# Optimization experiments

Hardware: AMD Instinct MI355X
Metric: run time of the kernel (lower is better)

The kernel has to match this reference:

```python
import jax, jax.numpy as jnp
import numpy as np

N, F, H, C = 50000, 128, 256, 40
E = 800000
L, J = 3, 2
TOT = 7  # sum_{i<L} J**i


def setup_inputs() -> dict:
    key = jax.random.key(0)
    ks = jax.random.split(key, 16)
    def rn(k, shape, scale):
        return jax.random.normal(k, shape, jnp.float32) * scale
    w = lambda k, shape: rn(k, shape, 1.0 / np.sqrt(shape[0]).astype(np.float32))
    return {
        "x": rn(ks[0], (N, F), 1.0),
        "feature": rn(ks[1], (TOT, N, F), 1.0),
        "src": jax.random.randint(ks[2], (E,), 0, N),
        "dst": jax.random.randint(ks[3], (E,), 0, N),
        "conv_W0": w(ks[4], (F, H)),       "conv_b0": jnp.zeros((H,), jnp.float32),
        "conv_W1": w(ks[5], (2 * H, H)),   "conv_b1": jnp.zeros((H,), jnp.float32),
        "conv_W2": w(ks[6], (2 * H, H)),   "conv_b2": jnp.zeros((H,), jnp.float32),
        "lin_W0": w(ks[7], (F, H)),        "lin_b0": jnp.zeros((H,), jnp.float32),
        "lin_W1": w(ks[8], (2 * F, H)),    "lin_b1": jnp.zeros((H,), jnp.float32),
        "lin_W2": w(ks[9], (4 * F, H)),    "lin_b2": jnp.zeros((H,), jnp.float32),
        "order_weights": rn(ks[10], (J,), 1.0 / np.sqrt(J).astype(np.float32)),
        "cls_W": w(ks[11], (2 * H, C)),    "cls_b": jnp.zeros((C,), jnp.float32),
    }


def reference(x, feature, src, dst,
              conv_W0, conv_b0, conv_W1, conv_b1, conv_W2, conv_b2,
              lin_W0, lin_b0, lin_W1, lin_b1, lin_W2, lin_b2,
              order_weights, cls_W, cls_b):
    # GCN normalization with self-loops (A-hat = D^-1/2 (A+I) D^-1/2)
    loop = jnp.arange(N, dtype=src.dtype)
    src_sl = jnp.concatenate([src, loop])   # [E+N]
    dst_sl = jnp.concatenate([dst, loop])
    deg = jax.ops.segment_sum(jnp.ones_like(dst_sl, jnp.float32), dst_sl, num_segments=N)
    dinv = jax.lax.rsqrt(deg)  # deg >= 1 thanks to self loops
    norm = dinv[src_sl] * dinv[dst_sl]      # [E+N]

    def gcn(h, W, b):
        m = h @ W                            # transform first (smaller gather)
        agg = jax.ops.segment_sum(m[src_sl] * norm[:, None], dst_sl, num_segments=N)
        return agg + b

    conv_W = [conv_W0, conv_W1, conv_W2]
    conv_b = [conv_b0, conv_b1, conv_b2]
    lin_W = [lin_W0, lin_W1, lin_W2]
    lin_b = [lin_b0, lin_b1, lin_b2]

    comb = x
    begin = 0
    for i in range(L):
        convx = jax.nn.relu(gcn(comb, conv_W[i], conv_b[i]))  # [N, H]
        count = J ** i
        lf = feature[begin:begin + count]                      # [count, N, F]
        if i > 0:
            ow = jnp.tile(order_weights, J ** (i - 1)).reshape(-1, 1, 1)
            lf = ow * lf
        lf = jnp.moveaxis(lf, 0, 1).reshape(N, count * F)      # [N, count*F]
        lin_sct = jax.nn.relu(lf @ lin_W[i] + lin_b[i])        # [N, H]
        comb = jnp.concatenate([lin_sct, convx], axis=-1)      # [N, 2H]
        begin += count
    logits = gcn(comb, cls_W, cls_b)                           # [N, C]
    return jax.nn.log_softmax(logits, axis=-1), logits
```

## Files before the change

### kernel.cpp

```cpp
#include <hip/hip_runtime.h>

#define DEVI __device__ __forceinline__

namespace {

constexpr int Nn = 50000;
constexpr int Ne = 800000;
constexpr int Fd = 128;
constexpr int Hd = 256;
constexpr int Cd = 40;
constexpr int NB = (Nn + 255) / 256;

typedef __attribute__((ext_vector_type(8))) short s16x8;
typedef __attribute__((ext_vector_type(8))) unsigned short u16x8;
typedef __attribute__((ext_vector_type(4))) float f32x4;

DEVI unsigned short f2bf(float f) {
  unsigned int u = __builtin_bit_cast(unsigned int, f);
  u += 0x7fffu + ((u >> 16) & 1u);
  return (unsigned short)(u >> 16);
}
DEVI float bf2f(unsigned short s) {
  return __builtin_bit_cast(float, ((unsigned int)s) << 16);
}

DEVI void gld_lds16(const void* gptr, void* lds_base) {
  const unsigned m0v =
      (unsigned)__builtin_amdgcn_readfirstlane((unsigned)(uintptr_t)lds_base);
  asm volatile("s_mov_b32 m0, %0\n\t"
               "global_load_lds_dwordx4 %1, off"
               :: "s"(m0v), "v"(gptr) : "memory");
}

DEVI void wt_one(const float* __restrict__ W, unsigned short* __restrict__ Wt,
                 int idx, int K, int H, const float* __restrict__ ow) {
  int c = idx / K, k = idx - c * K;
  int kt = k >> 6, c16 = (k >> 3) & 7, j = k & 7;
  int ksrc = (kt << 6) | ((c16 ^ (c & 7)) << 3) | j;
  float v = (c < H) ? W[(size_t)ksrc * H + c] : 0.0f;
  if (ow) v *= ow[(ksrc >> 7) & 1];
  Wt[idx] = f2bf(v);
}

constexpr int WTO0 = 0;
constexpr int WTO1 = WTO0 + 256 * 128;
constexpr int WTO2 = WTO1 + 256 * 512;
constexpr int WTO3 = WTO2 + 256 * 512;
constexpr int WTO4 = WTO3 + 256 * 128;
constexpr int WTO5 = WTO4 + 256 * 256;
constexpr int WTO6 = WTO5 + 256 * 512;
constexpr int WTO7 = WTO6 + 64 * 512;
constexpr int PREPTOT = WTO7 + Nn;

__global__ __launch_bounds__(256) void k_prep(
    const float* W0, const float* W1, const float* W2, const float* W3,
    const float* W4, const float* W5, const float* W6, const float* ow,
    unsigned short* T0, unsigned short* T1, unsigned short* T2, unsigned short* T3,
    unsigned short* T4, unsigned short* T5, unsigned short* T6, int* cnt) {
  int idx = blockIdx.x * 256 + threadIdx.x;
  if (idx >= PREPTOT) return;
  if (idx < WTO1)      wt_one(W0, T0, idx - WTO0, 128, 256, nullptr);
  else if (idx < WTO2) wt_one(W1, T1, idx - WTO1, 512, 256, nullptr);
  else if (idx < WTO3) wt_one(W2, T2, idx - WTO2, 512, 256, nullptr);
  else if (idx < WTO4) wt_one(W3, T3, idx - WTO3, 128, 256, nullptr);
  else if (idx < WTO5) wt_one(W4, T4, idx - WTO4, 256, 256, ow);
  else if (idx < WTO6) wt_one(W5, T5, idx - WTO5, 512, 256, ow);
  else if (idx < WTO7) wt_one(W6, T6, idx - WTO6, 512, 40, nullptr);
  else cnt[idx - WTO7] = 0;
}

__global__ void k_count(const int* __restrict__ dst, int* __restrict__ cnt) {
  int e = blockIdx.x * 256 + threadIdx.x;
  if (e < Ne) atomicAdd(&cnt[dst[e]], 1);
}

__global__ __launch_bounds__(256) void k_partial(const int* __restrict__ cnt,
                                                 int* __restrict__ partial) {
  __shared__ int red[256];
  const int t = threadIdx.x;
  const int i = blockIdx.x * 256 + t;
  red[t] = (i < Nn) ? cnt[i] + 1 : 0;
  __syncthreads();
#pragma unroll
  for (int off = 128; off; off >>= 1) {
    if (t < off) red[t] += red[t + off];
    __syncthreads();
  }
  if (t == 0) partial[blockIdx.x] = red[0];
}

__global__ __launch_bounds__(256) void k_scan_small(const int* __restrict__ partial,
                                                    int* __restrict__ poffs,
                                                    int* __restrict__ rowptr) {
  __shared__ int s[256];
  const int t = threadIdx.x;
  const int v = (t < NB) ? partial[t] : 0;
  s[t] = v;
  __syncthreads();
#pragma unroll
  for (int off = 1; off < 256; off <<= 1) {
    int add = (t >= off) ? s[t - off] : 0;
    __syncthreads();
    s[t] += add;
    __syncthreads();
  }
  if (t < NB) poffs[t] = s[t] - v;
  if (t == NB - 1) rowptr[Nn] = s[t];
}

__global__ __launch_bounds__(256) void k_rowptr(const int* __restrict__ cnt,
                                                const int* __restrict__ poffs,
                                                int* __restrict__ rowptr,
                                                int* __restrict__ cursor,
                                                float* __restrict__ dinv) {
  __shared__ int s[256];
  const int t = threadIdx.x;
  const int i = blockIdx.x * 256 + t;
  const int c = (i < Nn) ? cnt[i] + 1 : 0;
  s[t] = c;
  __syncthreads();
#pragma unroll
  for (int off = 1; off < 256; off <<= 1) {
    int add = (t >= off) ? s[t - off] : 0;
    __syncthreads();
    s[t] += add;
    __syncthreads();
  }
  if (i < Nn) {
    const int excl = s[t] - c + poffs[blockIdx.x];
    rowptr[i] = excl;
    cursor[i] = excl;
    dinv[i] = rsqrtf((float)c);
  }
}

__global__ void k_fill(const int* __restrict__ src, const int* __restrict__ dst,
                       const float* __restrict__ dinv, int* __restrict__ cursor,
                       int* __restrict__ csrs, float* __restrict__ csrn) {
  int e = blockIdx.x * 256 + threadIdx.x;
  if (e < Ne) {
    int s = src[e], d = dst[e];
    int pos = atomicAdd(&cursor[d], 1);
    csrs[pos] = s;
    csrn[pos] = dinv[s] * dinv[d];
  } else if (e < Ne + Nn) {
    int d = e - Ne;
    int pos = atomicAdd(&cursor[d], 1);
    csrs[pos] = d;
    float v = dinv[d];
    csrn[pos] = v * v;
  }
}

struct GRole {
  const float* A;
  const unsigned short* Wt;
  const float* bias;
  unsigned short* C;
  int K;
  int ldc;
  int relu;
};

__global__ __launch_bounds__(256) void k_gemm4(GRole R0, GRole R1, GRole R2, GRole R3) {
  const GRole R = (blockIdx.y == 0) ? R0 : (blockIdx.y == 1) ? R1
                  : (blockIdx.y == 2) ? R2 : R3;
  __shared__ char smem[81920];
  short* lA0 = (short*)smem;
  short* lA1 = (short*)(smem + 8192);
  short* lB0 = (short*)(smem + 16384);
  short* lB1 = (short*)(smem + 49152);
  const int tid = threadIdx.x;
  const int lane = tid & 63;
  const int wid = tid >> 6;
  const int wc = wid;
  const int row0 = blockIdx.x * 64;
  const size_t NnF = (size_t)Nn * Fd;

  f32x4 acc[4][4];
#pragma unroll
  for (int i = 0; i < 4; ++i)
#pragma unroll
    for (int j = 0; j < 4; ++j) acc[i][j] = (f32x4)0.0f;

  auto issueA = [&](int kt, f32x4 (&A4)[2][2]) {
    const int k0 = kt * 64;
    const int c = k0 >> 7;
    const int f0 = k0 & 127;
#pragma unroll
    for (int i = 0; i < 2; ++i) {
      const int v = tid * 2 + i;
      const int row = v >> 3, c16 = v & 7;
      const int grow = row0 + row;
      const bool rv = grow < Nn;
      const float* p = R.A + (size_t)c * NnF + (size_t)grow * Fd + f0 + c16 * 8;
      A4[i][0] = rv ? *(const f32x4*)p : (f32x4)0.0f;
      A4[i][1] = rv ? *(const f32x4*)(p + 4) : (f32x4)0.0f;
    }
  };
  auto writeA = [&](f32x4 (&A4)[2][2], short* lAb) {
#pragma unroll
    for (int i = 0; i < 2; ++i) {
      const int v = tid * 2 + i;
      const int row = v >> 3, c16 = v & 7;
      s16x8 val;
#pragma unroll
      for (int q = 0; q < 4; ++q) val[q] = (short)f2bf(A4[i][0][q]);
#pragma unroll
      for (int q = 0; q < 4; ++q) val[4 + q] = (short)f2bf(A4[i][1][q]);
      int byte = row * 128 + c16 * 16;
      byte ^= (row & 7) << 4;
      *(s16x8*)((char*)lAb + byte) = val;
    }
  };
  auto stageB = [&](int kt) {
    short* b = (kt & 1) ? lB1 : lB0;
    const int k0 = kt * 64;
#pragma unroll
    for (int i = 0; i < 8; ++i) {
      const int iss = wid * 8 + i;
      const int col = iss * 8 + (lane >> 3);
      gld_lds16(R.Wt + (size_t)col * R.K + k0 + (lane & 7) * 8, b + iss * 512);
    }
  };
  auto mfma = [&](const short* lAb, const short* lBb) {
#pragma unroll
    for (int kk = 0; kk < 2; ++kk) {
      s16x8 af[4], bv[4];
#pragma unroll
      for (int mi = 0; mi < 4; ++mi) {
        int r = mi * 16 + (lane & 15);
        int byte = r * 128 + kk * 64 + (lane >> 4) * 16;
        byte ^= (r & 7) << 4;
        af[mi] = *(const s16x8*)((const char*)lAb + byte);
      }
#pragma unroll
      for (int ni = 0; ni < 4; ++ni) {
        int c = wc * 64 + ni * 16 + (lane & 15);
        int byte = c * 128 + kk * 64 + (lane >> 4) * 16;
        byte ^= (c & 7) << 4;
        bv[ni] = *(const s16x8*)((const char*)lBb + byte);
      }
#pragma unroll
      for (int mi = 0; mi < 4; ++mi)
#pragma unroll
        for (int ni = 0; ni < 4; ++ni)
          acc[mi][ni] = __builtin_amdgcn_mfma_f32_16x16x32_bf16(af[mi], bv[ni], acc[mi][ni], 0, 0, 0);
    }
  };

  const int nkt = R.K >> 6;
  f32x4 Ar0[2][2], Ar1[2][2];
  issueA(0, Ar0);
  stageB(0);
  issueA(1, Ar1);
  stageB(1);
  for (int kt = 0; kt < nkt; ++kt) {
    short* curA = (kt & 1) ? lA1 : lA0;
    short* curB = (kt & 1) ? lB1 : lB0;
    if (kt & 1) writeA(Ar1, curA); else writeA(Ar0, curA);
    if (kt + 2 < nkt) {
      if (kt & 1) issueA(kt + 2, Ar1); else issueA(kt + 2, Ar0);
    }
    if (kt + 2 < nkt)      asm volatile("s_waitcnt vmcnt(16)" ::: "memory");
    else if (kt + 1 < nkt) asm volatile("s_waitcnt vmcnt(12)" ::: "memory");
    else                   asm volatile("s_waitcnt vmcnt(0)" ::: "memory");
    asm volatile("s_waitcnt lgkmcnt(0)" ::: "memory");
    __builtin_amdgcn_s_barrier();
    mfma(curA, curB);
    __builtin_amdgcn_s_barrier();
    if (kt + 2 < nkt) stageB(kt + 2);
  }

  short* lC = (short*)smem;
#pragma unroll
  for (int ni = 0; ni < 4; ++ni) {
    const int col = wc * 64 + ni * 16 + (lane & 15);
    const float bvl = R.bias ? R.bias[col] : 0.0f;
#pragma unroll
    for (int mi = 0; mi < 4; ++mi) {
      const int rb = mi * 16 + ((lane >> 4) << 2);
#pragma unroll
      for (int q = 0; q < 4; ++q) {
        float vv = acc[mi][ni][q] + bvl;
        if (R.relu) vv = fmaxf(vv, 0.0f);
        lC[(rb + q) * 264 + col] = f2bf(vv);
      }
    }
  }
  __syncthreads();
#pragma unroll
  for (int p = 0; p < 8; ++p) {
    const int flat = p * 256 + tid;
    const int row = flat >> 5;
    const int ch = flat & 31;
    const int r = row0 + row;
    if (r < Nn)
      *(u16x8*)(R.C + (size_t)r * R.ldc + ch * 8) =
          *(const u16x8*)(lC + row * 264 + ch * 8);
  }
}

__global__ __launch_bounds__(256) void k_gemmC(
    const unsigned short* __restrict__ A, int lda, int K,
    const unsigned short* __restrict__ Wt, unsigned short* __restrict__ C,
    int ldc) {
  __shared__ char smem[81920];
  short* lA0 = (short*)smem;
  short* lA1 = (short*)(smem + 8192);
  short* lB0 = (short*)(smem + 16384);
  short* lB1 = (short*)(smem + 49152);
  const int tid = threadIdx.x;
  const int lane = tid & 63;
  const int wid = tid >> 6;
  const int wc = wid;
  const int row0 = blockIdx.x * 64;
  const int c16a = (lane & 7) ^ ((lane >> 3) & 7);

  f32x4 acc[4][4];
#pragma unroll
  for (int i = 0; i < 4; ++i)
#pragma unroll
    for (int j = 0; j < 4; ++j) acc[i][j] = (f32x4)0.0f;

  auto stage = [&](int kt) {
    short* a = (kt & 1) ? lA1 : lA0;
    short* b = (kt & 1) ? lB1 : lB0;
    const int k0 = kt * 64;
#pragma unroll
    for (int i = 0; i < 2; ++i) {
      const int iss = wid * 2 + i;
      const int row = row0 + iss * 8 + (lane >> 3);
      gld_lds16(A + (size_t)row * lda + k0 + c16a * 8, a + iss * 512);
    }
#pragma unroll
    for (int i = 0; i < 8; ++i) {
      const int iss = wid * 8 + i;
      const int col = iss * 8 + (lane >> 3);
      gld_lds16(Wt + (size_t)col * K + k0 + (lane & 7) * 8, b + iss * 512);
    }
  };
  auto mfma = [&](const short* lAb, const short* lBb) {
#pragma unroll
    for (int kk = 0; kk < 2; ++kk) {
      s16x8 af[4], bv[4];
#pragma unroll
      for (int mi = 0; mi < 4; ++mi) {
        int r = mi * 16 + (lane & 15);
        int byte = r * 128 + kk * 64 + (lane >> 4) * 16;
        byte ^= (r & 7) << 4;
        af[mi] = *(const s16x8*)((const char*)lAb + byte);
      }
#pragma unroll
      for (int ni = 0; ni < 4; ++ni) {
        int c = wc * 64 + ni * 16 + (lane & 15);
        int byte = c * 128 + kk * 64 + (lane >> 4) * 16;
        byte ^= (c & 7) << 4;
        bv[ni] = *(const s16x8*)((const char*)lBb + byte);
      }
#pragma unroll
      for (int mi = 0; mi < 4; ++mi)
#pragma unroll
        for (int ni = 0; ni < 4; ++ni)
          acc[mi][ni] = __builtin_amdgcn_mfma_f32_16x16x32_bf16(af[mi], bv[ni], acc[mi][ni], 0, 0, 0);
    }
  };

  const int nkt = K >> 6;
  stage(0);
  stage(1);
  for (int kt = 0; kt < nkt; ++kt) {
    short* curA = (kt & 1) ? lA1 : lA0;
    short* curB = (kt & 1) ? lB1 : lB0;
    if (kt + 1 < nkt) asm volatile("s_waitcnt vmcnt(10)" ::: "memory");
    else              asm volatile("s_waitcnt vmcnt(0)" ::: "memory");
    __builtin_amdgcn_s_barrier();
    mfma(curA, curB);
    __builtin_amdgcn_s_barrier();
    if (kt + 2 < nkt) stage(kt + 2);
  }

  short* lC = (short*)smem;
#pragma unroll
  for (int ni = 0; ni < 4; ++ni) {
    const int col = wc * 64 + ni * 16 + (lane & 15);
#pragma unroll
    for (int mi = 0; mi < 4; ++mi) {
      const int rb = mi * 16 + ((lane >> 4) << 2);
#pragma unroll
      for (int q = 0; q < 4; ++q)
        lC[(rb + q) * 264 + col] = f2bf(acc[mi][ni][q]);
    }
  }
  __syncthreads();
#pragma unroll
  for (int p = 0; p < 8; ++p) {
    const int flat = p * 256 + tid;
    const int row = flat >> 5;
    const int ch = flat & 31;
    const int r = row0 + row;
    if (r < Nn)
      *(u16x8*)(C + (size_t)r * ldc + ch * 8) =
          *(const u16x8*)(lC + row * 264 + ch * 8);
  }
}

__global__ __launch_bounds__(256) void k_gemmX(
    const unsigned short* __restrict__ A, int lda, int K,
    const unsigned short* __restrict__ Wt, unsigned short* __restrict__ C,
    int ldc, int ncols) {
  __shared__ char smem[81920];
  short* lA0 = (short*)smem;
  short* lA1 = (short*)(smem + 32768);
  short* lB0 = (short*)(smem + 65536);
  short* lB1 = (short*)(smem + 73728);
  const int tid = threadIdx.x;
  const int lane = tid & 63;
  const int wid = tid >> 6;
  const int wr = wid;
  const int row0 = blockIdx.x * 256;
  const int c16a = (lane & 7) ^ ((lane >> 3) & 7);

  f32x4 acc[4][4];
#pragma unroll
  for (int i = 0; i < 4; ++i)
#pragma unroll
    for (int j = 0; j < 4; ++j) acc[i][j] = (f32x4)0.0f;

  auto stage = [&](int kt) {
    short* a = (kt & 1) ? lA1 : lA0;
    short* b = (kt & 1) ? lB1 : lB0;
    const int k0 = kt * 64;
#pragma unroll
    for (int i = 0; i < 8; ++i) {
      const int iss = wid * 8 + i;
      const int row = row0 + iss * 8 + (lane >> 3);
      gld_lds16(A + (size_t)row * lda + k0 + c16a * 8, a + iss * 512);
    }
#pragma unroll
    for (int i = 0; i < 2; ++i) {
      const int iss = wid * 2 + i;
      const int col = iss * 8 + (lane >> 3);
      gld_lds16(Wt + (size_t)col * K + k0 + (lane & 7) * 8, b + iss * 512);
    }
  };
  auto mfma = [&](const short* a, const short* b) {
#pragma unroll
    for (int kk = 0; kk < 2; ++kk) {
      s16x8 af[4], bv[4];
#pragma unroll
      for (int mi = 0; mi < 4; ++mi) {
        int r = wr * 64 + mi * 16 + (lane & 15);
        int byte = r * 128 + kk * 64 + (lane >> 4) * 16;
        byte ^= (r & 7) << 4;
        af[mi] = *(const s16x8*)((const char*)a + byte);
      }
#pragma unroll
      for (int ni = 0; ni < 4; ++ni) {
        int c = ni * 16 + (lane & 15);
        int byte = c * 128 + kk * 64 + (lane >> 4) * 16;
        byte ^= (c & 7) << 4;
        bv[ni] = *(const s16x8*)((const char*)b + byte);
      }
#pragma unroll
      for (int mi = 0; mi < 4; ++mi)
#pragma unroll
        for (int ni = 0; ni < 4; ++ni)
          acc[mi][ni] = __builtin_amdgcn_mfma_f32_16x16x32_bf16(af[mi], bv[ni], acc[mi][ni], 0, 0, 0);
    }
  };

  const int nkt = K >> 6;
  stage(0);
  stage(1);
  for (int kt = 0; kt < nkt; ++kt) {
    short* curA = (kt & 1) ? lA1 : lA0;
    short* curB = (kt & 1) ? lB1 : lB0;
    if (kt + 1 < nkt) asm volatile("s_waitcnt vmcnt(10)" ::: "memory");
    else              asm volatile("s_waitcnt vmcnt(0)" ::: "memory");
    __builtin_amdgcn_s_barrier();
    mfma(curA, curB);
    __builtin_amdgcn_s_barrier();
    if (kt + 2 < nkt) stage(kt + 2);
  }

  short* lC = (short*)smem;
#pragma unroll
  for (int ni = 0; ni < 4; ++ni) {
    const int col = ni * 16 + (lane & 15);
#pragma unroll
    for (int mi = 0; mi < 4; ++mi) {
      const int rb = wr * 64 + mi * 16 + ((lane >> 4) << 2);
#pragma unroll
      for (int q = 0; q < 4; ++q)
        lC[(rb + q) * 72 + col] = f2bf(acc[mi][ni][q]);
    }
  }
  __syncthreads();
#pragma unroll
  for (int p = 0; p < 8; ++p) {
    const int flat = p * 256 + tid;
    const int row = flat >> 3;
    const int ch = flat & 7;
    const int r = row0 + row;
    const int col = ch * 8;
    if (r < Nn && col < ncols)
      *(u16x8*)(C + (size_t)r * ldc + col) = *(const u16x8*)(lC + row * 72 + col);
  }
}

__global__ __launch_bounds__(256) void k_gather(
    const unsigned short* __restrict__ m, const int* __restrict__ rowptr,
    const int* __restrict__ csrs, const float* __restrict__ csrn,
    const float* __restrict__ bias, unsigned short* __restrict__ outp,
    int ldc, int col_off) {
  const int wid = (blockIdx.x * 256 + threadIdx.x) >> 6;
  const int lane = threadIdx.x & 63;
  if (wid >= Nn) return;
  const int half = lane >> 5;
  const int sub = lane & 31;
  const int e0 = rowptr[wid], e1 = rowptr[wid + 1];
  const unsigned short* mcol = m + sub * 8;
  float acc[8];
#pragma unroll
  for (int q = 0; q < 8; ++q) acc[q] = 0.f;

  for (int base = e0; base < e1; base += 64) {
    const int idx = base + lane;
    int s_ = 0;
    float w_ = 0.f;
    if (idx < e1) { s_ = csrs[idx]; w_ = csrn[idx]; }
    const int cn = min(64, e1 - base);
    const int npair = (cn + 1) >> 1;
    float w0, w1, w2, w3;
    u16x8 v0, v1, v2, v3;
    auto pick = [&](int p, float& w, u16x8& v) {
      if (p < npair) {
        const int j = 2 * p + half;
        const int ss = __shfl(s_, j);
        w = __shfl(w_, j);
        v = *(const u16x8*)(mcol + (size_t)ss * Hd);
      } else { w = 0.f; v = (u16x8)0; }
    };
    pick(0, w0, v0); pick(1, w1, v1); pick(2, w2, v2); pick(3, w3, v3);
    for (int p0 = 0; p0 < npair; p0 += 4) {
#pragma unroll
      for (int q = 0; q < 8; ++q) acc[q] += w0 * bf2f(v0[q]);
      pick(p0 + 4, w0, v0);
#pragma unroll
      for (int q = 0; q < 8; ++q) acc[q] += w1 * bf2f(v1[q]);
      pick(p0 + 5, w1, v1);
#pragma unroll
      for (int q = 0; q < 8; ++q) acc[q] += w2 * bf2f(v2[q]);
      pick(p0 + 6, w2, v2);
#pragma unroll
      for (int q = 0; q < 8; ++q) acc[q] += w3 * bf2f(v3[q]);
      pick(p0 + 7, w3, v3);
    }
  }

#pragma unroll
  for (int q = 0; q < 8; ++q) acc[q] += __shfl_xor(acc[q], 32);
  if (half == 0) {
    u16x8 o;
#pragma unroll
    for (int q = 0; q < 8; ++q) {
      float v = fmaxf(acc[q] + bias[sub * 8 + q], 0.f);
      o[q] = f2bf(v);
    }
    *(u16x8*)(outp + (size_t)wid * ldc + col_off + sub * 8) = o;
  }
}

__global__ __launch_bounds__(256) void k_gcls(
    const unsigned short* __restrict__ mc, const int* __restrict__ rowptr,
    const int* __restrict__ csrs, const float* __restrict__ csrn,
    const float* __restrict__ clsb, float* __restrict__ outp) {
  const int wid = (blockIdx.x * 256 + threadIdx.x) >> 6;
  const int lane = threadIdx.x & 63;
  if (wid >= Nn) return;
  const int half = lane >> 5;
  const int sub = lane & 31;
  const bool act = sub < 5;
  const int e0 = rowptr[wid], e1 = rowptr[wid + 1];
  float acc[8];
#pragma unroll
  for (int q = 0; q < 8; ++q) acc[q] = 0.f;

  for (int base = e0; base < e1; base += 64) {
    const int idx = base + lane;
    int s_ = 0;
    float w_ = 0.f;
    if (idx < e1) { s_ = csrs[idx]; w_ = csrn[idx]; }
    const int cn = min(64, e1 - base);
    const int npair = (cn + 1) >> 1;
    int sA = __shfl(s_, half);
    float wA = __shfl(w_, half);
    u16x8 vA = act ? *(const u16x8*)(mc + (size_t)sA * Cd + sub * 8) : (u16x8)0;
    for (int jj = 1; jj < npair; ++jj) {
      const int j = 2 * jj + half;
      const int sB = __shfl(s_, j);
      const float wB = __shfl(w_, j);
      const u16x8 vB = act ? *(const u16x8*)(mc + (size_t)sB * Cd + sub * 8) : (u16x8)0;
#pragma unroll
      for (int q = 0; q < 8; ++q) acc[q] += wA * bf2f(vA[q]);
      wA = wB; vA = vB;
    }
#pragma unroll
    for (int q = 0; q < 8; ++q) acc[q] += wA * bf2f(vA[q]);
  }

#pragma unroll
  for (int q = 0; q < 8; ++q) acc[q] += __shfl_xor(acc[q], 32);

  float l[8];
  float mx = -3.4e38f;
  if (act) {
#pragma unroll
    for (int q = 0; q < 8; ++q) {
      l[q] = acc[q] + clsb[sub * 8 + q];
      mx = fmaxf(mx, l[q]);
    }
  }
#pragma unroll
  for (int off = 1; off < 8; off <<= 1) mx = fmaxf(mx, __shfl_xor(mx, off));
  float se = 0.f;
  if (act) {
#pragma unroll
    for (int q = 0; q < 8; ++q) se += expf(l[q] - mx);
  }
#pragma unroll
  for (int off = 1; off < 8; off <<= 1) se += __shfl_xor(se, off);
  const float lse = mx + logf(se);
  if (half == 0 && act) {
    float* o1 = outp + (size_t)wid * Cd + sub * 8;
    float* o2 = o1 + (size_t)Nn * Cd;
#pragma unroll
    for (int q = 0; q < 8; ++q) {
      o1[q] = l[q] - lse;
      o2[q] = l[q];
    }
  }
}

}

extern "C" void kernel_launch(void* const* d_in, const int* in_sizes, int n_in,
                              void* d_out, int out_size, void* d_ws, size_t ws_size,
                              hipStream_t stream) {
  (void)in_sizes; (void)n_in; (void)out_size; (void)ws_size;
  const float* x       = (const float*)d_in[0];
  const float* feature = (const float*)d_in[1];
  const int* src       = (const int*)d_in[2];
  const int* dst       = (const int*)d_in[3];
  const float* convW[3] = {(const float*)d_in[4], (const float*)d_in[6], (const float*)d_in[8]};
  const float* convB[3] = {(const float*)d_in[5], (const float*)d_in[7], (const float*)d_in[9]};
  const float* linW[3]  = {(const float*)d_in[10], (const float*)d_in[12], (const float*)d_in[14]};
  const float* linB[3]  = {(const float*)d_in[11], (const float*)d_in[13], (const float*)d_in[15]};
  const float* oweights = (const float*)d_in[16];
  const float* clsW     = (const float*)d_in[17];
  const float* clsB     = (const float*)d_in[18];
  float* out = (float*)d_out;

  char* wsp = (char*)d_ws;
  auto alloc = [&](size_t bytes) -> void* {
    void* p = wsp;
    wsp += (bytes + 255) & ~(size_t)255;
    return p;
  };
  int* cnt      = (int*)alloc((size_t)Nn * 4);
  int* cursor   = (int*)alloc((size_t)Nn * 4);
  int* rowptr   = (int*)alloc((size_t)(Nn + 1) * 4);
  float* dinv   = (float*)alloc((size_t)Nn * 4);
  int* partial  = (int*)alloc((size_t)NB * 4);
  int* poffs    = (int*)alloc((size_t)NB * 4);
  int* csrs     = (int*)alloc((size_t)(Ne + Nn) * 4);
  float* csrn   = (float*)alloc((size_t)(Ne + Nn) * 4);
  unsigned short* WtC0 = (unsigned short*)alloc((size_t)256 * 128 * 2);
  unsigned short* WtC1 = (unsigned short*)alloc((size_t)256 * 512 * 2);
  unsigned short* WtC2 = (unsigned short*)alloc((size_t)256 * 512 * 2);
  unsigned short* WtL0 = (unsigned short*)alloc((size_t)256 * 128 * 2);
  unsigned short* WtL1 = (unsigned short*)alloc((size_t)256 * 256 * 2);
  unsigned short* WtL2 = (unsigned short*)alloc((size_t)256 * 512 * 2);
  unsigned short* WtCl = (unsigned short*)alloc((size_t)64 * 512 * 2);
  unsigned short* mbuf = (unsigned short*)alloc((size_t)Nn * Hd * 2);
  unsigned short* mcls = (unsigned short*)alloc((size_t)Nn * Cd * 2);
  unsigned short* comb0 = (unsigned short*)alloc((size_t)(Nn + 256) * 512 * 2);
  unsigned short* comb1 = (unsigned short*)alloc((size_t)(Nn + 256) * 512 * 2);
  unsigned short* comb2 = (unsigned short*)alloc((size_t)(Nn + 256) * 512 * 2);

  k_prep<<<(PREPTOT + 255) / 256, 256, 0, stream>>>(
      convW[0], convW[1], convW[2], linW[0], linW[1], linW[2], clsW, oweights,
      WtC0, WtC1, WtC2, WtL0, WtL1, WtL2, WtCl, cnt);
  k_count<<<(Ne + 255) / 256, 256, 0, stream>>>(dst, cnt);
  k_partial<<<NB, 256, 0, stream>>>(cnt, partial);
  k_scan_small<<<1, 256, 0, stream>>>(partial, poffs, rowptr);
  k_rowptr<<<NB, 256, 0, stream>>>(cnt, poffs, rowptr, cursor, dinv);
  k_fill<<<(Ne + Nn + 255) / 256, 256, 0, stream>>>(src, dst, dinv, cursor, csrs, csrn);

  const int GM = (Nn + 63) / 64;
  const int GC = (Nn + 255) / 256;
  const int GB = (Nn * 64) / 256;

  GRole rConv0{x,                              WtC0, nullptr, mbuf,  128, Hd,  0};
  GRole rLin0 {feature,                        WtL0, linB[0], comb0, 128, 512, 1};
  GRole rLin1 {feature + (size_t)1 * Nn * Fd,  WtL1, linB[1], comb1, 256, 512, 1};
  GRole rLin2 {feature + (size_t)3 * Nn * Fd,  WtL2, linB[2], comb2, 512, 512, 1};
  k_gemm4<<<dim3(GM, 4), 256, 0, stream>>>(rConv0, rLin0, rLin1, rLin2);

  k_gather<<<GB, 256, 0, stream>>>(mbuf, rowptr, csrs, csrn, convB[0], comb0, 512, 256);
  k_gemmC<<<GM, 256, 0, stream>>>(comb0, 512, 512, WtC1, mbuf, Hd);
  k_gather<<<GB, 256, 0, stream>>>(mbuf, rowptr, csrs, csrn, convB[1], comb1, 512, 256);
  k_gemmC<<<GM, 256, 0, stream>>>(comb1, 512, 512, WtC2, mbuf, Hd);
  k_gather<<<GB, 256, 0, stream>>>(mbuf, rowptr, csrs, csrn, convB[2], comb2, 512, 256);
  k_gemmX<<<GC, 256, 0, stream>>>(comb2, 512, 512, WtCl, mcls, Cd, 40);
  k_gcls<<<GB, 256, 0, stream>>>(mcls, rowptr, csrs, csrn, clsB, out);
}
```

Before: 480.6 us.

## Single-buffer B in GEMM with register prefetch and one barrier per k-step

After: 486.2 us. Within noise of the previous version (+1.2%).

```diff
diff --git a/kernel.cpp b/kernel.cpp
--- a/kernel.cpp
+++ b/kernel.cpp
@@ -14,6 +14,7 @@
 typedef __attribute__((ext_vector_type(8))) short s16x8;
 typedef __attribute__((ext_vector_type(8))) unsigned short u16x8;
 typedef __attribute__((ext_vector_type(4))) float f32x4;
+typedef __attribute__((ext_vector_type(4))) unsigned int u32x4;
 
 DEVI unsigned short f2bf(float f) {
   unsigned int u = __builtin_bit_cast(unsigned int, f);
@@ -22,6 +23,11 @@
 }
 DEVI float bf2f(unsigned short s) {
   return __builtin_bit_cast(float, ((unsigned int)s) << 16);
+}
+DEVI unsigned cvtpk(float lo, float hi) {
+  unsigned r;
+  asm("v_cvt_pk_bf16_f32 %0, %1, %2" : "=v"(r) : "v"(lo), "v"(hi));
+  return r;
 }
 
 DEVI void gld_lds16(const void* gptr, void* lds_base) {
@@ -165,11 +171,10 @@
 __global__ __launch_bounds__(256) void k_gemm4(GRole R0, GRole R1, GRole R2, GRole R3) {
   const GRole R = (blockIdx.y == 0) ? R0 : (blockIdx.y == 1) ? R1
                   : (blockIdx.y == 2) ? R2 : R3;
-  __shared__ char smem[81920];
+  __shared__ char smem[49152];
   short* lA0 = (short*)smem;
   short* lA1 = (short*)(smem + 8192);
-  short* lB0 = (short*)(smem + 16384);
-  short* lB1 = (short*)(smem + 49152);
+  short* lB  = (short*)(smem + 16384);
   const int tid = threadIdx.x;
   const int lane = tid & 63;
   const int wid = tid >> 6;
@@ -203,30 +208,40 @@
     for (int i = 0; i < 2; ++i) {
       const int v = tid * 2 + i;
       const int row = v >> 3, c16 = v & 7;
-      s16x8 val;
-#pragma unroll
-      for (int q = 0; q < 4; ++q) val[q] = (short)f2bf(A4[i][0][q]);
-#pragma unroll
-      for (int q = 0; q < 4; ++q) val[4 + q] = (short)f2bf(A4[i][1][q]);
+      u32x4 val;
+      val.x = cvtpk(A4[i][0][0], A4[i][0][1]);
+      val.y = cvtpk(A4[i][0][2], A4[i][0][3]);
+      val.z = cvtpk(A4[i][1][0], A4[i][1][1]);
+      val.w = cvtpk(A4[i][1][2], A4[i][1][3]);
       int byte = row * 128 + c16 * 16;
       byte ^= (row & 7) << 4;
-      *(s16x8*)((char*)lAb + byte) = val;
+      *(u32x4*)((char*)lAb + byte) = val;
     }
   };
   auto stageB = [&](int kt) {
-    short* b = (kt & 1) ? lB1 : lB0;
     const int k0 = kt * 64;
 #pragma unroll
     for (int i = 0; i < 8; ++i) {
       const int iss = wid * 8 + i;
       const int col = iss * 8 + (lane >> 3);
-      gld_lds16(R.Wt + (size_t)col * R.K + k0 + (lane & 7) * 8, b + iss * 512);
-    }
-  };
-  auto mfma = [&](const short* lAb, const short* lBb) {
+      gld_lds16(R.Wt + (size_t)col * R.K + k0 + (lane & 7) * 8, lB + iss * 512);
+    }
+  };
+  auto readB = [&](s16x8 (&bv)[2][4]) {
+#pragma unroll
+    for (int kk = 0; kk < 2; ++kk)
+#pragma unroll
+      for (int ni = 0; ni < 4; ++ni) {
+        int c = wc * 64 + ni * 16 + (lane & 15);
+        int byte = c * 128 + kk * 64 + (lane >> 4) * 16;
+        byte ^= (c & 7) << 4;
+        bv[kk][ni] = *(const s16x8*)((const char*)lB + byte);
+      }
+  };
+  auto mfma = [&](const short* lAb, s16x8 (&bv)[2][4]) {
 #pragma unroll
     for (int kk = 0; kk < 2; ++kk) {
-      s16x8 af[4], bv[4];
+      s16x8 af[4];
 #pragma unroll
       for (int mi = 0; mi < 4; ++mi) {
         int r = mi * 16 + (lane & 15);
@@ -235,17 +250,10 @@
         af[mi] = *(const s16x8*)((const char*)lAb + byte);
       }
 #pragma unroll
-      for (int ni = 0; ni < 4; ++ni) {
-        int c = wc * 64 + ni * 16 + (lane & 15);
-        int byte = c * 128 + kk * 64 + (lane >> 4) * 16;
-        byte ^= (c & 7) << 4;
-        bv[ni] = *(const s16x8*)((const char*)lBb + byte);
-      }
-#pragma unroll
       for (int mi = 0; mi < 4; ++mi)
 #pragma unroll
         for (int ni = 0; ni < 4; ++ni)
-          acc[mi][ni] = __builtin_amdgcn_mfma_f32_16x16x32_bf16(af[mi], bv[ni], acc[mi][ni], 0, 0, 0);
+          acc[mi][ni] = __builtin_amdgcn_mfma_f32_16x16x32_bf16(af[mi], bv[kk][ni], acc[mi][ni], 0, 0, 0);
     }
   };
 
@@ -254,22 +262,25 @@
   issueA(0, Ar0);
   stageB(0);
   issueA(1, Ar1);
-  stageB(1);
+  writeA(Ar0, lA0);
+  asm volatile("s_waitcnt lgkmcnt(0)" ::: "memory");
+  __builtin_amdgcn_s_barrier();
   for (int kt = 0; kt < nkt; ++kt) {
-    short* curA = (kt & 1) ? lA1 : lA0;
-    short* curB = (kt & 1) ? lB1 : lB0;
-    if (kt & 1) writeA(Ar1, curA); else writeA(Ar0, curA);
+    if (kt + 1 < nkt) asm volatile("s_waitcnt vmcnt(4)" ::: "memory");
+    else              asm volatile("s_waitcnt vmcnt(0)" ::: "memory");
+    s16x8 bv[2][4];
+    readB(bv);
+    asm volatile("s_waitcnt lgkmcnt(0)" ::: "memory");
+    if (kt + 1 < nkt) stageB(kt + 1);
     if (kt + 2 < nkt) {
       if (kt & 1) issueA(kt + 2, Ar1); else issueA(kt + 2, Ar0);
     }
-    if (kt + 2 < nkt)      asm volatile("s_waitcnt vmcnt(16)" ::: "memory");
-    else if (kt + 1 < nkt) asm volatile("s_waitcnt vmcnt(12)" ::: "memory");
-    else                   asm volatile("s_waitcnt vmcnt(0)" ::: "memory");
+    if (kt + 1 < nkt) {
+      if ((kt + 1) & 1) writeA(Ar1, lA1); else writeA(Ar0, lA0);
+    }
+    mfma((kt & 1) ? lA1 : lA0, bv);
     asm volatile("s_waitcnt lgkmcnt(0)" ::: "memory");
     __builtin_amdgcn_s_barrier();
-    mfma(curA, curB);
-    __builtin_amdgcn_s_barrier();
-    if (kt + 2 < nkt) stageB(kt + 2);
   }
 
   short* lC = (short*)smem;
```
